# Optimization experiments

Hardware: AMD Instinct MI355X
Metric: run time of the kernel (lower is better)

Reference implementation:

```python
import jax, jax.numpy as jnp
import numpy as np

B, S, D, H, NUM_LABELS = 16, 1024, 1024, 16, 3
LN_EPS = 1e-5


def setup_inputs() -> dict:
    key = jax.random.key(0)
    ks = iter(jax.random.split(key, 16))

    def w(shape, k):
        return jax.random.normal(k, shape, jnp.float32) * 0.02

    inp = {}
    inp["embedded"] = jax.random.normal(next(ks), (B, S, D), jnp.float32)
    inp["attention_mask"] = jnp.ones((B, S), jnp.float32)
    for pfx in ("p2h", "h2p"):
        for name in ("q", "k", "v", "o"):
            inp[f"{pfx}_W{name}"] = w((D, D), next(ks))
            inp[f"{pfx}_b{name}"] = jnp.zeros((D,), jnp.float32)
        inp[f"{pfx}_ln_g"] = jnp.ones((D,), jnp.float32)
        inp[f"{pfx}_ln_b"] = jnp.zeros((D,), jnp.float32)
    inp["W1"] = w((4 * D, D), next(ks)); inp["b1"] = jnp.zeros((D,), jnp.float32)
    inp["W2"] = w((D, D // 2), next(ks)); inp["b2"] = jnp.zeros((D // 2,), jnp.float32)
    inp["W3"] = w((D // 2, NUM_LABELS), next(ks)); inp["b3"] = jnp.zeros((NUM_LABELS,), jnp.float32)
    return inp


def _layernorm(x, g, b):
    mu = jnp.mean(x, axis=-1, keepdims=True)
    var = jnp.mean(jnp.square(x - mu), axis=-1, keepdims=True)
    return (x - mu) / jnp.sqrt(var + LN_EPS) * g + b


def _cross_attn(q_in, kv_in, kv_mask, Wq, bq, Wk, bk, Wv, bv, Wo, bo, g, bln):
    Bs, Sq, Dm = q_in.shape
    Sk = kv_in.shape[1]
    hd = Dm // H
    Q = (q_in @ Wq + bq).reshape(Bs, Sq, H, hd)
    K = (kv_in @ Wk + bk).reshape(Bs, Sk, H, hd)
    V = (kv_in @ Wv + bv).reshape(Bs, Sk, H, hd)
    scores = jnp.einsum("bqhd,bkhd->bhqk", Q, K) / jnp.sqrt(jnp.float32(hd))
    scores = jnp.where(kv_mask[:, None, None, :] == 0, jnp.float32(-1e9), scores)
    wts = jax.nn.softmax(scores, axis=-1)  # dropout is identity in eval
    att = jnp.einsum("bhqk,bkhd->bqhd", wts, V).reshape(Bs, Sq, Dm)
    return _layernorm(att @ Wo + bo + q_in, g, bln)


def _pool(x, m):
    s = jnp.sum(x * m[:, :, None], axis=1)
    d = jnp.clip(jnp.sum(m, axis=1, keepdims=True), 1e-9, None)
    return s / d


def reference(embedded, attention_mask,
              p2h_Wq, p2h_bq, p2h_Wk, p2h_bk, p2h_Wv, p2h_bv, p2h_Wo, p2h_bo, p2h_ln_g, p2h_ln_b,
              h2p_Wq, h2p_bq, h2p_Wk, h2p_bk, h2p_Wv, h2p_bv, h2p_Wo, h2p_bo, h2p_ln_g, h2p_ln_b,
              W1, b1, W2, b2, W3, b3):
    half = embedded.shape[1] // 2
    premise, hypothesis = embedded[:, :half], embedded[:, half:]
    pm, hm = attention_mask[:, :half], attention_mask[:, half:]
    p2h = _cross_attn(premise, hypothesis, hm,
                      p2h_Wq, p2h_bq, p2h_Wk, p2h_bk, p2h_Wv, p2h_bv, p2h_Wo, p2h_bo, p2h_ln_g, p2h_ln_b)
    h2p = _cross_attn(hypothesis, premise, pm,
                      h2p_Wq, h2p_bq, h2p_Wk, h2p_bk, h2p_Wv, h2p_bv, h2p_Wo, h2p_bo, h2p_ln_g, h2p_ln_b)
    feats = jnp.concatenate([_pool(premise, pm), _pool(hypothesis, hm),
                             _pool(p2h, pm), _pool(h2p, hm)], axis=-1)
    h1 = jax.nn.relu(feats @ W1 + b1)
    h2 = jax.nn.relu(h1 @ W2 + b2)
    return h2 @ W3 + b3
```

## Files before the change

kernel.cpp:

```cpp
#include <hip/hip_runtime.h>
#include <hip/hip_bf16.h>

typedef __attribute__((ext_vector_type(8))) __bf16 bf16x8;
typedef __attribute__((ext_vector_type(4))) float f32x4;
typedef __attribute__((ext_vector_type(4))) int i32x4;
typedef __attribute__((ext_vector_type(4))) unsigned short u16x4;

#define MFMA16(a, b, c) __builtin_amdgcn_mfma_f32_16x16x32_bf16((a), (b), (c), 0, 0, 0)

__device__ __forceinline__ void gload_lds16(const void* g, void* l)
{
    __builtin_amdgcn_global_load_lds(
        (const __attribute__((address_space(1))) unsigned int*)g,
        (__attribute__((address_space(3))) unsigned int*)l, 16, 0, 0);
}

__global__ __launch_bounds__(256) void cast_emb_kernel(const float* __restrict__ emb,
                                                       __bf16* __restrict__ Pb,
                                                       __bf16* __restrict__ Hb)
{
    int i = (blockIdx.x * 256 + threadIdx.x) * 4;
    int r = i >> 10, d = i & 1023;
    size_t src = ((size_t)(r >> 9) * 1024 + (r & 511)) * 1024 + d;
    f32x4 p = *(const f32x4*)(emb + src);
    f32x4 h = *(const f32x4*)(emb + src + 512 * 1024);
    union { __bf16 b[4]; u16x4 u; } cp, ch;
#pragma unroll
    for (int j = 0; j < 4; ++j) { cp.b[j] = (__bf16)p[j]; ch.b[j] = (__bf16)h[j]; }
    *(u16x4*)(Pb + i) = cp.u;
    *(u16x4*)(Hb + i) = ch.u;
}

struct WPtrs { const float* p[8]; };
__global__ __launch_bounds__(256) void cast_wt_kernel(WPtrs wp, __bf16* __restrict__ Wt0)
{
    const float* W = wp.p[blockIdx.z];
    __bf16* Wt = Wt0 + (size_t)blockIdx.z * 1048576;
    __shared__ float tile[32][33];
    int n0 = blockIdx.x * 32, k0 = blockIdx.y * 32;
    int tx = threadIdx.x, ty = threadIdx.y;
#pragma unroll
    for (int i = ty; i < 32; i += 8)
        tile[i][tx] = W[(size_t)(k0 + i) * 1024 + n0 + tx];
    __syncthreads();
#pragma unroll
    for (int i = ty; i < 32; i += 8)
        Wt[(size_t)(n0 + i) * 1024 + k0 + tx] = (__bf16)tile[tx][i];
}

template <int EPI>
__global__ __launch_bounds__(256, 3) void gemm_bt(const __bf16* __restrict__ A,
                                                  const __bf16* __restrict__ Bt,
                                                  const float* __restrict__ bias,
                                                  const float* __restrict__ bias2,
                                                  __bf16* __restrict__ Cb,
                                                  __bf16* __restrict__ Cb2,
                                                  float* __restrict__ Cf,
                                                  const float* __restrict__ resid,
                                                  int resid_half, int M, int N, int K)
{
    __shared__ __align__(16) __bf16 As[128 * 32];
    __shared__ __align__(16) __bf16 Bs[128 * 32];
    const int t = threadIdx.x;
    const int l = t & 63, w = t >> 6;
    const int wr = w >> 1, wc = w & 1;
    const int lrow = l & 15, lk = l >> 4;
    const int m0 = blockIdx.y * 128, n0 = blockIdx.x * 128;
    const int r0 = t >> 2, kc0 = (t & 3) * 8;

    const __bf16* gA0 = A + (size_t)(m0 + r0) * K + kc0;
    const __bf16* gA1 = gA0 + (size_t)64 * K;
    const __bf16* gB0 = Bt + (size_t)(n0 + r0) * K + kc0;
    const __bf16* gB1 = gB0 + (size_t)64 * K;
    __bf16* dA0 = &As[r0 * 32 + kc0];
    __bf16* dA1 = &As[(r0 + 64) * 32 + kc0];
    __bf16* dB0 = &Bs[r0 * 32 + kc0];
    __bf16* dB1 = &Bs[(r0 + 64) * 32 + kc0];

    const f32x4 zero = {0.f, 0.f, 0.f, 0.f};
    f32x4 acc[4][4];
#pragma unroll
    for (int mi = 0; mi < 4; ++mi)
#pragma unroll
        for (int ni = 0; ni < 4; ++ni) acc[mi][ni] = zero;

    const int nk = K >> 5;
    for (int kt = 0; kt < nk; ++kt) {
        const int ko = kt * 32;
        gload_lds16(gA0 + ko, dA0);
        gload_lds16(gA1 + ko, dA1);
        gload_lds16(gB0 + ko, dB0);
        gload_lds16(gB1 + ko, dB1);
        __syncthreads();
        bf16x8 af[4], bfv[4];
#pragma unroll
        for (int mi = 0; mi < 4; ++mi)
            af[mi] = *(const bf16x8*)(&As[(wr * 64 + mi * 16 + lrow) * 32 + lk * 8]);
#pragma unroll
        for (int ni = 0; ni < 4; ++ni)
            bfv[ni] = *(const bf16x8*)(&Bs[(wc * 64 + ni * 16 + lrow) * 32 + lk * 8]);
#pragma unroll
        for (int mi = 0; mi < 4; ++mi)
#pragma unroll
            for (int ni = 0; ni < 4; ++ni)
                acc[mi][ni] = MFMA16(af[mi], bfv[ni], acc[mi][ni]);
        __syncthreads();
    }

#pragma unroll
    for (int mi = 0; mi < 4; ++mi) {
#pragma unroll
        for (int ni = 0; ni < 4; ++ni) {
            int col = n0 + wc * 64 + ni * 16 + lrow;
            float bv = (EPI == 3 && col >= 1024) ? bias2[col - 1024] : bias[col];
#pragma unroll
            for (int r = 0; r < 4; ++r) {
                int row = m0 + wr * 64 + mi * 16 + lk * 4 + r;
                float v = acc[mi][ni][r] + bv;
                if (EPI == 0) {
                    Cb[(size_t)row * N + col] = (__bf16)v;
                } else if (EPI == 3) {
                    if (col < 1024) {
                        Cb[(size_t)row * 1024 + col] = (__bf16)v;
                    } else {
                        int c2 = col - 1024;
                        int b_ = row >> 9, pos = row & 511;
                        int h_ = c2 >> 6, hd = c2 & 63;
                        Cb2[(((size_t)(b_ * 16 + h_) * 64 + hd) << 9) + pos] = (__bf16)v;
                    }
                } else {
                    int b_ = row >> 9, s = row & 511;
                    float rv = resid[((size_t)b_ * 1024 + resid_half + s) * 1024 + col];
                    Cf[(size_t)row * N + col] = v + rv;
                }
            }
        }
    }
}

__global__ __launch_bounds__(256, 2) void attn_kernel(const __bf16* __restrict__ Q,
                                                      const __bf16* __restrict__ Kb,
                                                      const __bf16* __restrict__ Vt,
                                                      const float* __restrict__ mask,
                                                      int mask_half,
                                                      __bf16* __restrict__ att)
{
    __shared__ __align__(16) __bf16 KP[512 * 64];
    __shared__ __align__(16) float msk[512];
    const int bh = blockIdx.x, b = bh >> 4, h = bh & 15;
    const int q0 = blockIdx.y * 64;
    const int t = threadIdx.x, l = t & 63, w = t >> 6;
    const int lrow = l & 15, lk = l >> 4;
    char* KPc = (char*)KP;

#pragma unroll
    for (int i = 0; i < 16; ++i) {
        int c = t + i * 256;
        int pos = c >> 3, slot = c & 7;
        *(i32x4*)(KPc + pos * 128 + ((slot ^ (pos & 7)) << 4)) =
            *(const i32x4*)(&Kb[((size_t)(b * 512 + pos)) * 1024 + h * 64 + slot * 8]);
    }
    for (int i = t; i < 512; i += 256) msk[i] = mask[b * 1024 + mask_half + i];

    const int qrow = q0 + w * 16 + lrow;
    const __bf16* qptr = Q + ((size_t)(b * 512 + qrow)) * 1024 + h * 64;
    bf16x8 qf0 = *(const bf16x8*)(qptr + lk * 8);
    bf16x8 qf1 = *(const bf16x8*)(qptr + 32 + lk * 8);
    __syncthreads();

    const f32x4 zero = {0.f, 0.f, 0.f, 0.f};
    f32x4 sc[32];
#pragma unroll
    for (int j = 0; j < 32; ++j) {
        const char* kb = KPc + (j * 16 + lrow) * 128;
        bf16x8 k0 = *(const bf16x8*)(kb + ((lk ^ (lrow & 7)) << 4));
        bf16x8 k1 = *(const bf16x8*)(kb + (((lk + 4) ^ (lrow & 7)) << 4));
        f32x4 c = zero;
        c = MFMA16(k0, qf0, c);
        c = MFMA16(k1, qf1, c);
        sc[j] = c;
    }

    float mx = -3e38f;
#pragma unroll
    for (int j = 0; j < 32; ++j) {
        f32x4 mv = *(const f32x4*)(&msk[j * 16 + lk * 4]);
#pragma unroll
        for (int r = 0; r < 4; ++r) {
            float s = sc[j][r] * 0.125f;
            if (mv[r] == 0.f) s = -1e9f;
            sc[j][r] = s;
            mx = fmaxf(mx, s);
        }
    }
    mx = fmaxf(mx, __shfl_xor(mx, 16));
    mx = fmaxf(mx, __shfl_xor(mx, 32));
    float sm = 0.f;
#pragma unroll
    for (int j = 0; j < 32; ++j)
#pragma unroll
        for (int r = 0; r < 4; ++r) {
            float e = __expf(sc[j][r] - mx);
            sc[j][r] = e;
            sm += e;
        }
    sm += __shfl_xor(sm, 16);
    sm += __shfl_xor(sm, 32);
    const float inv = 1.f / sm;

    __syncthreads();
    const int prow = w * 16 + lrow;
    char* prowp = KPc + prow * 1024;
    const int psw = (prow & 7);
#pragma unroll
    for (int j = 0; j < 32; ++j) {
        union { __bf16 b[4]; unsigned long long u; } pk;
#pragma unroll
        for (int r = 0; r < 4; ++r) pk.b[r] = (__bf16)(sc[j][r] * inv);
        int slot = j * 2 + (lk >> 1);
        *(unsigned long long*)(prowp + (((slot ^ psw) << 4) | ((lk & 1) * 8))) = pk.u;
    }

    const __bf16* vsrc = Vt + (size_t)bh * 64 * 512;
    f32x4 av[4];
#pragma unroll
    for (int ni = 0; ni < 4; ++ni) av[ni] = zero;
#pragma unroll
    for (int ks = 0; ks < 16; ++ks) {
        bf16x8 pf = *(const bf16x8*)(prowp + (((ks * 4 + lk) ^ psw) << 4));
#pragma unroll
        for (int ni = 0; ni < 4; ++ni) {
            bf16x8 vf = *(const bf16x8*)(&vsrc[(ni * 16 + lrow) * 512 + ks * 32 + lk * 8]);
            av[ni] = MFMA16(pf, vf, av[ni]);
        }
    }
#pragma unroll
    for (int ni = 0; ni < 4; ++ni)
#pragma unroll
        for (int r = 0; r < 4; ++r) {
            int qq = q0 + w * 16 + lk * 4 + r;
            att[((size_t)(b * 512 + qq)) * 1024 + h * 64 + ni * 16 + lrow] =
                (__bf16)av[ni][r];
        }
}

__global__ __launch_bounds__(256) void ln_kernel(const float* __restrict__ X,
                                                 const float* __restrict__ g,
                                                 const float* __restrict__ bta,
                                                 __bf16* __restrict__ out)
{
    const int r = blockIdx.x, t = threadIdx.x;
    const float* x = X + (size_t)r * 1024;
    f32x4 v = *(const f32x4*)(x + t * 4);
    float s = v[0] + v[1] + v[2] + v[3];
    float q = v[0] * v[0] + v[1] * v[1] + v[2] * v[2] + v[3] * v[3];
#pragma unroll
    for (int d = 1; d < 64; d <<= 1) { s += __shfl_xor(s, d); q += __shfl_xor(q, d); }
    __shared__ float rs[4], rq[4];
    if ((t & 63) == 0) { rs[t >> 6] = s; rq[t >> 6] = q; }
    __syncthreads();
    s = rs[0] + rs[1] + rs[2] + rs[3];
    q = rq[0] + rq[1] + rq[2] + rq[3];
    float mu = s * (1.f / 1024.f);
    float var = q * (1.f / 1024.f) - mu * mu;
    float rstd = rsqrtf(var + 1e-5f);
#pragma unroll
    for (int j = 0; j < 4; ++j) {
        int c = t * 4 + j;
        out[(size_t)r * 1024 + c] = (__bf16)((v[j] - mu) * rstd * g[c] + bta[c]);
    }
}

__global__ __launch_bounds__(256) void pool_f32_kernel(const float* __restrict__ X,
                                                       const float* __restrict__ mask,
                                                       float* __restrict__ feats)
{
    const int b = blockIdx.y, d0 = blockIdx.x * 64, half = blockIdx.z * 512;
    const int t = threadIdx.x, d = d0 + (t & 63), sl = t >> 6;
    float acc = 0.f, ms = 0.f;
#pragma unroll 4
    for (int s = sl * 128; s < sl * 128 + 128; ++s) {
        float m = mask[b * 1024 + half + s];
        acc += X[((size_t)b * 1024 + half + s) * 1024 + d] * m;
        ms += m;
    }
    __shared__ float ra[4][64];
    __shared__ float rm[4];
    ra[sl][t & 63] = acc;
    if ((t & 63) == 0) rm[sl] = ms;
    __syncthreads();
    if (t < 64) {
        float a = ra[0][t] + ra[1][t] + ra[2][t] + ra[3][t];
        float m = rm[0] + rm[1] + rm[2] + rm[3];
        feats[b * 4096 + blockIdx.z * 1024 + d0 + t] = a / fmaxf(m, 1e-9f);
    }
}

__global__ __launch_bounds__(256) void pool_bf16_kernel(const __bf16* __restrict__ X,
                                                        const float* __restrict__ mask,
                                                        int half, float* __restrict__ feats,
                                                        int off)
{
    const int b = blockIdx.y, d0 = blockIdx.x * 64;
    const int t = threadIdx.x, d = d0 + (t & 63), sl = t >> 6;
    float acc = 0.f, ms = 0.f;
#pragma unroll 4
    for (int s = sl * 128; s < sl * 128 + 128; ++s) {
        float m = mask[b * 1024 + half + s];
        acc += (float)X[((size_t)b * 512 + s) * 1024 + d] * m;
        ms += m;
    }
    __shared__ float ra[4][64];
    __shared__ float rm[4];
    ra[sl][t & 63] = acc;
    if ((t & 63) == 0) rm[sl] = ms;
    __syncthreads();
    if (t < 64) {
        float a = ra[0][t] + ra[1][t] + ra[2][t] + ra[3][t];
        float m = rm[0] + rm[1] + rm[2] + rm[3];
        feats[b * 4096 + off + d0 + t] = a / fmaxf(m, 1e-9f);
    }
}

__global__ __launch_bounds__(256) void fc_init_kernel(const float* __restrict__ b1,
                                                      const float* __restrict__ b2,
                                                      float* __restrict__ h1,
                                                      float* __restrict__ h2)
{
    int i = blockIdx.x * 256 + threadIdx.x;
    if (i < 16 * 1024) h1[i] = b1[i & 1023];
    else h2[i - 16 * 1024] = b2[(i - 16 * 1024) & 511];
}

template <int CH, int RELU_IN>
__global__ __launch_bounds__(256) void fc_atomic_kernel(const float* __restrict__ in,
                                                        const float* __restrict__ W,
                                                        float* __restrict__ out,
                                                        int IF, int OF)
{
    __shared__ float ins[16 * CH];
    const int t = threadIdx.x;
    const int col = blockIdx.x * 256 + t;
    const int i0 = blockIdx.y * CH;
#pragma unroll
    for (int idx = t; idx < 16 * CH; idx += 256) {
        int b = idx / CH, i = idx % CH;
        float v = in[b * IF + i0 + i];
        if (RELU_IN) v = fmaxf(v, 0.f);
        ins[idx] = v;
    }
    __syncthreads();
    float acc[16];
#pragma unroll
    for (int b = 0; b < 16; ++b) acc[b] = 0.f;
#pragma unroll 4
    for (int i = 0; i < CH; ++i) {
        float wv = W[(size_t)(i0 + i) * OF + col];
#pragma unroll
        for (int b = 0; b < 16; ++b) acc[b] += ins[b * CH + i] * wv;
    }
#pragma unroll
    for (int b = 0; b < 16; ++b) atomicAdd(out + b * OF + col, acc[b]);
}

__global__ __launch_bounds__(64) void mlp3_kernel(const float* __restrict__ h2,
                                                  const float* __restrict__ W3,
                                                  const float* __restrict__ b3,
                                                  float* __restrict__ out)
{
    int b = blockIdx.x, t = threadIdx.x;
    float a0 = 0.f, a1 = 0.f, a2 = 0.f;
    for (int i = t; i < 512; i += 64) {
        float hv = fmaxf(h2[b * 512 + i], 0.f);
        a0 += hv * W3[i * 3 + 0];
        a1 += hv * W3[i * 3 + 1];
        a2 += hv * W3[i * 3 + 2];
    }
#pragma unroll
    for (int d = 1; d < 64; d <<= 1) {
        a0 += __shfl_xor(a0, d);
        a1 += __shfl_xor(a1, d);
        a2 += __shfl_xor(a2, d);
    }
    if (t == 0) {
        out[b * 3 + 0] = a0 + b3[0];
        out[b * 3 + 1] = a1 + b3[1];
        out[b * 3 + 2] = a2 + b3[2];
    }
}

extern "C" void kernel_launch(void* const* d_in, const int* in_sizes, int n_in,
                              void* d_out, int out_size, void* d_ws, size_t ws_size,
                              hipStream_t stream)
{
    const float* emb  = (const float*)d_in[0];
    const float* mask = (const float*)d_in[1];
    const float* W1 = (const float*)d_in[22];
    const float* b1 = (const float*)d_in[23];
    const float* W2 = (const float*)d_in[24];
    const float* b2 = (const float*)d_in[25];
    const float* W3 = (const float*)d_in[26];
    const float* b3 = (const float*)d_in[27];

    char* ws = (char*)d_ws;
    constexpr size_t MB = 1ull << 20;
    __bf16* Pb    = (__bf16*)(ws);
    __bf16* Hb    = (__bf16*)(ws + 16 * MB);
    __bf16* Wt    = (__bf16*)(ws + 32 * MB);
    __bf16* Qb    = (__bf16*)(ws + 48 * MB);
    __bf16* Kb    = (__bf16*)(ws + 64 * MB);
    __bf16* Vt    = (__bf16*)(ws + 80 * MB);
    __bf16* attb  = (__bf16*)(ws + 96 * MB);
    float*  Of    = (float*) (ws + 48 * MB);
    __bf16* ctx   = (__bf16*)(ws + 112 * MB);
    float*  feats = (float*) (ws + 128 * MB);
    float*  h1    = (float*) (ws + 128 * MB + 512 * 1024);
    float*  h2    = (float*) (ws + 129 * MB);

    cast_emb_kernel<<<8192, 256, 0, stream>>>(emb, Pb, Hb);
    WPtrs wp;
    const int widx[8] = {2, 4, 6, 8, 12, 14, 16, 18};
    for (int i = 0; i < 8; ++i) wp.p[i] = (const float*)d_in[widx[i]];
    cast_wt_kernel<<<dim3(32, 32, 8), dim3(32, 8), 0, stream>>>(wp, Wt);

    dim3 gg(8, 64);
    dim3 gkv(16, 64);
    for (int dir = 0; dir < 2; ++dir) {
        const __bf16* qin  = dir ? Hb : Pb;
        const __bf16* kvin = dir ? Pb : Hb;
        const int base = dir ? 12 : 2;
        const __bf16* wq  = Wt + (size_t)(dir * 4 + 0) * 1048576;
        const __bf16* wkv = Wt + (size_t)(dir * 4 + 1) * 1048576;
        const __bf16* wo  = Wt + (size_t)(dir * 4 + 3) * 1048576;
        const float* bq  = (const float*)d_in[base + 1];
        const float* bk  = (const float*)d_in[base + 3];
        const float* bv  = (const float*)d_in[base + 5];
        const float* bo  = (const float*)d_in[base + 7];
        const float* lng = (const float*)d_in[base + 8];
        const float* lnb = (const float*)d_in[base + 9];
        const int kvhalf  = dir ? 0 : 512;
        const int reshalf = dir ? 512 : 0;

        gemm_bt<0><<<gg, 256, 0, stream>>>(qin, wq, bq, nullptr, Qb, nullptr,
                                           nullptr, nullptr, 0, 8192, 1024, 1024);
        gemm_bt<3><<<gkv, 256, 0, stream>>>(kvin, wkv, bk, bv, Kb, Vt,
                                            nullptr, nullptr, 0, 8192, 2048, 1024);
        attn_kernel<<<dim3(256, 8), 256, 0, stream>>>(Qb, Kb, Vt, mask, kvhalf, attb);
        gemm_bt<2><<<gg, 256, 0, stream>>>(attb, wo, bo, nullptr, nullptr, nullptr,
                                           Of, emb, reshalf, 8192, 1024, 1024);
        ln_kernel<<<8192, 256, 0, stream>>>(Of, lng, lnb, ctx);
        pool_bf16_kernel<<<dim3(16, 16), 256, 0, stream>>>(ctx, mask, dir ? 512 : 0,
                                                           feats, 2048 + dir * 1024);
    }
    pool_f32_kernel<<<dim3(16, 16, 2), 256, 0, stream>>>(emb, mask, feats);

    fc_init_kernel<<<96, 256, 0, stream>>>(b1, b2, h1, h2);
    fc_atomic_kernel<128, 0><<<dim3(4, 32), 256, 0, stream>>>(feats, W1, h1, 4096, 1024);
    fc_atomic_kernel<32, 1><<<dim3(2, 32), 256, 0, stream>>>(h1, W2, h2, 1024, 512);
    mlp3_kernel<<<16, 64, 0, stream>>>(h2, W3, b3, (float*)d_out);
}
```

Measured before the change: 580.3 us.

## Split attention keys into two online-softmax tiles to halve LDS and registers

```diff
diff --git a/kernel.cpp b/kernel.cpp
--- a/kernel.cpp
+++ b/kernel.cpp
@@ -138,14 +138,14 @@
     }
 }
 
-__global__ __launch_bounds__(256, 2) void attn_kernel(const __bf16* __restrict__ Q,
+__global__ __launch_bounds__(256, 4) void attn_kernel(const __bf16* __restrict__ Q,
                                                       const __bf16* __restrict__ Kb,
                                                       const __bf16* __restrict__ Vt,
                                                       const float* __restrict__ mask,
                                                       int mask_half,
                                                       __bf16* __restrict__ att)
 {
-    __shared__ __align__(16) __bf16 KP[512 * 64];
+    __shared__ __align__(16) __bf16 KP[256 * 64];
     __shared__ __align__(16) float msk[512];
     const int bh = blockIdx.x, b = bh >> 4, h = bh & 15;
     const int q0 = blockIdx.y * 64;
@@ -153,12 +153,14 @@
     const int lrow = l & 15, lk = l >> 4;
     char* KPc = (char*)KP;
 
-#pragma unroll
-    for (int i = 0; i < 16; ++i) {
+    const __bf16* kbase = Kb + ((size_t)b * 512) * 1024 + h * 64;
+    const __bf16* vsrc = Vt + (size_t)bh * 64 * 512;
+
+#pragma unroll
+    for (int i = 0; i < 8; ++i) {
         int c = t + i * 256;
-        int pos = c >> 3, slot = c & 7;
-        *(i32x4*)(KPc + pos * 128 + ((slot ^ (pos & 7)) << 4)) =
-            *(const i32x4*)(&Kb[((size_t)(b * 512 + pos)) * 1024 + h * 64 + slot * 8]);
+        int pos = c >> 3, gslot = (c & 7) ^ (pos & 7);
+        gload_lds16(kbase + (size_t)pos * 1024 + gslot * 8, KPc + c * 16);
     }
     for (int i = t; i < 512; i += 256) msk[i] = mask[b * 1024 + mask_half + i];
 
@@ -166,82 +168,115 @@
     const __bf16* qptr = Q + ((size_t)(b * 512 + qrow)) * 1024 + h * 64;
     bf16x8 qf0 = *(const bf16x8*)(qptr + lk * 8);
     bf16x8 qf1 = *(const bf16x8*)(qptr + 32 + lk * 8);
-    __syncthreads();
 
     const f32x4 zero = {0.f, 0.f, 0.f, 0.f};
-    f32x4 sc[32];
-#pragma unroll
-    for (int j = 0; j < 32; ++j) {
-        const char* kb = KPc + (j * 16 + lrow) * 128;
-        bf16x8 k0 = *(const bf16x8*)(kb + ((lk ^ (lrow & 7)) << 4));
-        bf16x8 k1 = *(const bf16x8*)(kb + (((lk + 4) ^ (lrow & 7)) << 4));
-        f32x4 c = zero;
-        c = MFMA16(k0, qf0, c);
-        c = MFMA16(k1, qf1, c);
-        sc[j] = c;
-    }
-
-    float mx = -3e38f;
-#pragma unroll
-    for (int j = 0; j < 32; ++j) {
-        f32x4 mv = *(const f32x4*)(&msk[j * 16 + lk * 4]);
+    f32x4 av[4];
+#pragma unroll
+    for (int ni = 0; ni < 4; ++ni) av[ni] = zero;
+    float m_run = -3e38f, su = 0.f;
+    const int psw = lrow & 7;
+    char* prowp = KPc + (w * 16 + lrow) * 512;
+    f32x4 sc[16];
+
+    auto qk_tile = [&]() {
+#pragma unroll
+        for (int jj = 0; jj < 16; ++jj) {
+            const char* kb = KPc + (jj * 16 + lrow) * 128;
+            bf16x8 k0 = *(const bf16x8*)(kb + ((lk ^ psw) << 4));
+            bf16x8 k1 = *(const bf16x8*)(kb + (((lk + 4) ^ psw) << 4));
+            f32x4 c = zero;
+            c = MFMA16(k0, qf0, c);
+            c = MFMA16(k1, qf1, c);
+            sc[jj] = c;
+        }
+    };
+
+    auto process_tile = [&](int koff) {
+        float mt = -3e38f;
+#pragma unroll
+        for (int jj = 0; jj < 16; ++jj) {
+            f32x4 mv = *(const f32x4*)(&msk[koff + jj * 16 + lk * 4]);
+#pragma unroll
+            for (int r = 0; r < 4; ++r) {
+                float s = sc[jj][r] * 0.125f;
+                if (mv[r] == 0.f) s = -1e9f;
+                sc[jj][r] = s;
+                mt = fmaxf(mt, s);
+            }
+        }
+        mt = fmaxf(mt, __shfl_xor(mt, 16));
+        mt = fmaxf(mt, __shfl_xor(mt, 32));
+        float m_new = fmaxf(m_run, mt);
+        float f = __expf(m_run - m_new);
+        float ssum = 0.f;
+#pragma unroll
+        for (int jj = 0; jj < 16; ++jj)
+#pragma unroll
+            for (int r = 0; r < 4; ++r) {
+                float e = __expf(sc[jj][r] - m_new);
+                sc[jj][r] = e;
+                ssum += e;
+            }
+        ssum += __shfl_xor(ssum, 16);
+        ssum += __shfl_xor(ssum, 32);
+        su = su * f + ssum;
+        m_run = m_new;
 #pragma unroll
         for (int r = 0; r < 4; ++r) {
-            float s = sc[j][r] * 0.125f;
-            if (mv[r] == 0.f) s = -1e9f;
-            sc[j][r] = s;
-            mx = fmaxf(mx, s);
-        }
-    }
-    mx = fmaxf(mx, __shfl_xor(mx, 16));
-    mx = fmaxf(mx, __shfl_xor(mx, 32));
-    float sm = 0.f;
-#pragma unroll
-    for (int j = 0; j < 32; ++j)
-#pragma unroll
-        for (int r = 0; r < 4; ++r) {
-            float e = __expf(sc[j][r] - mx);
-            sc[j][r] = e;
-            sm += e;
-        }
-    sm += __shfl_xor(sm, 16);
-    sm += __shfl_xor(sm, 32);
-    const float inv = 1.f / sm;
-
-    __syncthreads();
-    const int prow = w * 16 + lrow;
-    char* prowp = KPc + prow * 1024;
-    const int psw = (prow & 7);
-#pragma unroll
-    for (int j = 0; j < 32; ++j) {
-        union { __bf16 b[4]; unsigned long long u; } pk;
-#pragma unroll
-        for (int r = 0; r < 4; ++r) pk.b[r] = (__bf16)(sc[j][r] * inv);
-        int slot = j * 2 + (lk >> 1);
-        *(unsigned long long*)(prowp + (((slot ^ psw) << 4) | ((lk & 1) * 8))) = pk.u;
-    }
-
-    const __bf16* vsrc = Vt + (size_t)bh * 64 * 512;
-    f32x4 av[4];
-#pragma unroll
-    for (int ni = 0; ni < 4; ++ni) av[ni] = zero;
-#pragma unroll
-    for (int ks = 0; ks < 16; ++ks) {
-        bf16x8 pf = *(const bf16x8*)(prowp + (((ks * 4 + lk) ^ psw) << 4));
-#pragma unroll
-        for (int ni = 0; ni < 4; ++ni) {
-            bf16x8 vf = *(const bf16x8*)(&vsrc[(ni * 16 + lrow) * 512 + ks * 32 + lk * 8]);
-            av[ni] = MFMA16(pf, vf, av[ni]);
-        }
-    }
-#pragma unroll
-    for (int ni = 0; ni < 4; ++ni)
-#pragma unroll
-        for (int r = 0; r < 4; ++r) {
-            int qq = q0 + w * 16 + lk * 4 + r;
+            float fr = __shfl(f, (l & 48) | (lk * 4 + r));
+#pragma unroll
+            for (int ni = 0; ni < 4; ++ni) av[ni][r] *= fr;
+        }
+    };
+
+    auto pv_tile = [&](int koff) {
+#pragma unroll
+        for (int jj = 0; jj < 16; ++jj) {
+            union { __bf16 b[4]; unsigned long long u; } pk;
+#pragma unroll
+            for (int r = 0; r < 4; ++r) pk.b[r] = (__bf16)sc[jj][r];
+            int slot = jj * 2 + (lk >> 1);
+            *(unsigned long long*)(prowp + (((slot ^ psw) << 4) | ((lk & 1) << 3))) = pk.u;
+        }
+#pragma unroll
+        for (int ks = 0; ks < 8; ++ks) {
+            bf16x8 pf = *(const bf16x8*)(prowp + (((ks * 4 + lk) ^ psw) << 4));
+#pragma unroll
+            for (int ni = 0; ni < 4; ++ni) {
+                bf16x8 vf = *(const bf16x8*)(&vsrc[(ni * 16 + lrow) * 512 + koff + ks * 32 + lk * 8]);
+                av[ni] = MFMA16(pf, vf, av[ni]);
+            }
+        }
+    };
+
+    __syncthreads();
+    qk_tile();
+    process_tile(0);
+    __syncthreads();
+    pv_tile(0);
+    __syncthreads();
+#pragma unroll
+    for (int i = 0; i < 8; ++i) {
+        int c = t + i * 256;
+        int pos = c >> 3, gslot = (c & 7) ^ (pos & 7);
+        gload_lds16(kbase + (size_t)(256 + pos) * 1024 + gslot * 8, KPc + c * 16);
+    }
+    __syncthreads();
+    qk_tile();
+    process_tile(256);
+    __syncthreads();
+    pv_tile(256);
+
+    const float inv = 1.f / su;
+#pragma unroll
+    for (int r = 0; r < 4; ++r) {
+        float ivr = __shfl(inv, (l & 48) | (lk * 4 + r));
+        int qq = q0 + w * 16 + lk * 4 + r;
+#pragma unroll
+        for (int ni = 0; ni < 4; ++ni)
             att[((size_t)(b * 512 + qq)) * 1024 + h * 64 + ni * 16 + lrow] =
-                (__bf16)av[ni][r];
-        }
+                (__bf16)(av[ni][r] * ivr);
+    }
 }
 
 __global__ __launch_bounds__(256) void ln_kernel(const float* __restrict__ X,
```

Result: slower. 647.6 us (+11.6%).
